# Kernel optimization log

Hardware: AMD Instinct MI355X
Metric: run time of the kernel (lower is better)

## Reference

```python
import jax, jax.numpy as jnp
import numpy as np
from jax import lax


def setup_inputs() -> dict:
    key = jax.random.key(0)
    ks = jax.random.split(key, 8)
    B, H, W = 1, 128, 128

    def rnd(k, shape, fan_in):
        return jax.random.normal(k, shape, dtype=jnp.float32) / np.float32(np.sqrt(fan_in))

    return {
        "x": jax.random.normal(ks[0], (B, 1, H, W), dtype=jnp.float32),
        "z": jax.random.uniform(ks[1], (B, 1), dtype=jnp.float32),
        "w_conv1": rnd(ks[2], (16, 1, 9, 9), 81),
        "b_conv1": jnp.zeros((16,), jnp.float32),
        "w_conv2": rnd(ks[3], (16, 16, 5, 5), 16 * 25),
        "b_conv2": jnp.zeros((16,), jnp.float32),
        "w_fc1": rnd(ks[4], (1024, 128), 1024),
        "b_fc1": jnp.zeros((128,), jnp.float32),
        "w_pose": rnd(ks[5], (1, 16), 1),
        "b_pose": jnp.zeros((16,), jnp.float32),
        "w_fc2": rnd(ks[6], (144, 1), 144),
        "b_fc2": jnp.zeros((1,), jnp.float32),
    }


_DN = ("NCHW", "OIHW", "NCHW")  # conv dimension numbers
_P = 32  # GQ-CNN patch size


def _maxpool2(h):
    return lax.reduce_window(h, -jnp.inf, lax.max, (1, 1, 2, 2), (1, 1, 2, 2), "VALID")


def _gqcnn(patches, z_rep, w_conv1, b_conv1, w_conv2, b_conv2,
           w_fc1, b_fc1, w_pose, b_pose, w_fc2, b_fc2):
    # patches: [N,1,32,32], z_rep: [N,1] -> quality [N,1]
    h = jax.nn.relu(lax.conv_general_dilated(patches, w_conv1, (1, 1), "SAME",
                                             dimension_numbers=_DN)
                    + b_conv1[None, :, None, None])
    h = _maxpool2(h)  # [N,16,16,16]
    h = jax.nn.relu(lax.conv_general_dilated(h, w_conv2, (1, 1), "SAME",
                                             dimension_numbers=_DN)
                    + b_conv2[None, :, None, None])
    h = _maxpool2(h)  # [N,16,8,8]
    flat = h.reshape(h.shape[0], -1)  # [N,1024]
    f = jax.nn.relu(flat @ w_fc1 + b_fc1)      # [N,128]
    p = jax.nn.relu(z_rep @ w_pose + b_pose)   # [N,16]
    return jnp.concatenate([f, p], axis=1) @ w_fc2 + b_fc2  # [N,1]


def reference(x, z, w_conv1, b_conv1, w_conv2, b_conv2,
              w_fc1, b_fc1, w_pose, b_pose, w_fc2, b_fc2):
    B, _, H, W = x.shape
    Hp, Wp = H - _P, W - _P  # loop ranges in the original: range(H-32), range(W-32)
    # Batched patch extraction replaces the O(H*W) Python loop.
    pat = lax.conv_general_dilated_patches(x, (_P, _P), (1, 1), "VALID")  # [B,1024,H-31,W-31]
    pat = pat[:, :, :Hp, :Wp]
    pat = jnp.transpose(pat, (0, 2, 3, 1)).reshape(B * Hp * Wp, 1, _P, _P)
    z_rep = jnp.repeat(z, Hp * Wp, axis=0)  # matches [B,Hp,Wp] flattening order
    q = _gqcnn(pat, z_rep, w_conv1, b_conv1, w_conv2, b_conv2,
               w_fc1, b_fc1, w_pose, b_pose, w_fc2, b_fc2)  # [N,1]
    half = _P // 2
    heat = jnp.zeros_like(x).at[:, :, half:H - half, half:W - half].set(
        q.reshape(B, 1, Hp, Wp))
    return heat
```

## Files before the change

kernel.cpp:

```cpp
#include <hip/hip_runtime.h>

typedef __attribute__((ext_vector_type(8))) short short8;
typedef __attribute__((ext_vector_type(4))) float f32x4;
typedef unsigned short u16;

__device__ __forceinline__ u16 f2bf(float f) {
    unsigned u = __builtin_bit_cast(unsigned, f);
    unsigned r = u + 0x7fffu + ((u >> 16) & 1u);
    return (u16)(r >> 16);
}
__device__ __forceinline__ unsigned pkbf(float lo, float hi) {
    unsigned r;
    asm("v_cvt_pk_bf16_f32 %0, %1, %2" : "=v"(r) : "v"(lo), "v"(hi));
    return r;
}

__global__ __launch_bounds__(256) void k0_prep(
    const float* __restrict__ z, const float* __restrict__ w1,
    const float* __restrict__ w2, const float* __restrict__ wfc1,
    const float* __restrict__ wpose, const float* __restrict__ bpose,
    const float* __restrict__ wfc2, const float* __restrict__ bfc2,
    float* __restrict__ out, u16* __restrict__ w1p, u16* __restrict__ w2p,
    u16* __restrict__ fc1T, float* __restrict__ cst)
{
    int gt = blockIdx.x * 256 + threadIdx.x;
    out[gt] = 0.f;

    if (gt < 2560) {
        int l = (gt >> 3) & 63, j = gt & 7, s = gt >> 9;
        int o = l & 15, bq = l >> 4;
        u16 v = 0;
        if (bq < 3) {
            int dx = bq * 4 + (j & 3);
            int dy = -1;
            if (s < 4) dy = 2 * s + (j >> 2);
            else if (j < 4) dy = 8;
            if (dy >= 0 && dx <= 8) v = f2bf(w1[o * 81 + dy * 9 + dx]);
        }
        w1p[gt] = v;
    }
    if (gt < 6656) {
        int l = (gt >> 3) & 63, j = gt & 7, s = gt >> 9;
        int o = l & 15, bq = l >> 4;
        int dy, dx, c8; bool valid = true;
        if (s < 5)       { dy = s;     dx = bq >> 1;       c8 = bq & 1; }
        else if (s < 10) { dy = s - 5; dx = 2 + (bq >> 1); c8 = bq & 1; }
        else { dy = (s - 10) + 3 * (bq & 1); dx = 4; c8 = bq >> 1; valid = (dy <= 4); }
        int ci = c8 * 8 + j;
        w2p[gt] = valid ? f2bf(w2[o * 400 + ci * 25 + dy * 5 + dx]) : (u16)0;
    }
    {
        int base = gt * 8;
        int n = base >> 10, kk = base & 1023;
        short8 v;
        #pragma unroll
        for (int j = 0; j < 8; ++j) v[j] = (short)f2bf(wfc1[(kk + j) * 128 + n]);
        *(short8*)&fc1T[base] = v;
    }
    if (gt == 0) {
        float zz = z[0];
        float s = bfc2[0];
        for (int j = 0; j < 16; ++j) {
            float p = fmaxf(zz * wpose[j] + bpose[j], 0.f);
            s += p * wfc2[128 + j];
        }
        *cst = s;
    }
}

__global__ __launch_bounds__(256, 4) void k1_feat(
    const float* __restrict__ x, const u16* __restrict__ w1p,
    const u16* __restrict__ w2p, const float* __restrict__ b1g,
    const float* __restrict__ b2g, u16* __restrict__ feat)
{
    __shared__ unsigned s2[40 * 44];
    __shared__ u16 s_h1p[20 * 20 * 24];
    __shared__ unsigned s_feat[512];

    const int tid = threadIdx.x;
    const int lane = tid & 63;
    const int wv = tid >> 6;
    const int mm = lane & 15;
    const int bq = lane >> 4;
    const int blk = blockIdx.x;
    const int py = blk / 96, px = blk % 96;

    {
        uint4 z4 = {0, 0, 0, 0};
        for (int i = tid; i < 152; i += 256) {
            int dst;
            if (i < 88) { int r8 = i / 11, c4 = i % 11;
                          int row = (r8 < 4) ? r8 : 32 + r8; dst = row * 11 + c4; }
            else        { int j = i - 88; dst = (4 + (j >> 1)) * 11 + 9 + (j & 1); }
            ((uint4*)s2)[dst] = z4;
        }
        for (int i = tid; i < 1728; i += 256) {
            int yx, d;
            if (i < 960) { int r = i / 240, off = i - r * 240;
                           int y = (r < 2) ? r : 16 + r;
                           yx = y * 20 + off / 12; d = off % 12; }
            else { int j = i - 960; int yy = 2 + j / 48; int rest = j % 48;
                   int xs = rest / 12; d = rest % 12;
                   int xx = (xs < 2) ? xs : 16 + xs; yx = yy * 20 + xx; }
            ((unsigned*)s_h1p)[yx * 12 + d] = 0;
        }
    }

    short8 w1f[5], w2f[13];
    #pragma unroll
    for (int s = 0; s < 5; ++s) w1f[s] = *(const short8*)&w1p[(s * 64 + lane) * 8];
    #pragma unroll
    for (int s = 0; s < 13; ++s) w2f[s] = *(const short8*)&w2p[(s * 64 + lane) * 8];
    const float bias1 = b1g[mm], bias2 = b2g[mm];

    for (int task = tid; task < 288; task += 256) {
        int ir = task / 9, g = task - ir * 9;
        int ic0 = g * 4 - 4;
        const float* xr = x + (py + ir) * 128 + px;
        float v[5];
        #pragma unroll
        for (int vi = 0; vi < 5; ++vi) {
            int ic = ic0 + vi;
            v[vi] = (ic >= 0 && ic < 32) ? xr[ic] : 0.f;
        }
        uint4 w;
        w.x = pkbf(v[0], v[1]);
        w.y = pkbf(v[1], v[2]);
        w.z = pkbf(v[2], v[3]);
        w.w = pkbf(v[3], v[4]);
        *(uint4*)&s2[(4 + ir) * 44 + g * 4] = w;
    }
    __syncthreads();

    union F { short8 s; unsigned u[4]; };
    const int dxq = (bq == 3) ? 0 : bq;

    for (int qi = 0; qi < 4; ++qi) {
        int q = wv + qi * 4;
        for (int h = 0; h < 2; ++h) {
            const unsigned* pb = &s2[(2 * q) * 44 + h * 16 + mm + dxq * 4];
            f32x4 accA = {0, 0, 0, 0}, accB = {0, 0, 0, 0};
            #pragma unroll
            for (int s = 0; s < 5; ++s) {
                F a, b;
                const unsigned* ra = pb + 2 * s * 44;
                a.u[0] = ra[0];  a.u[1] = ra[2];
                a.u[2] = ra[44]; a.u[3] = ra[46];
                const int blo = (s < 4) ? (2 * s + 1) * 44 : 9 * 44;
                const int bhi = (s < 4) ? (2 * s + 2) * 44 : 8 * 44;
                b.u[0] = pb[blo];     b.u[1] = pb[blo + 2];
                b.u[2] = pb[bhi];     b.u[3] = pb[bhi + 2];
                accA = __builtin_amdgcn_mfma_f32_16x16x32_bf16(a.s, w1f[s], accA, 0, 0, 0);
                accB = __builtin_amdgcn_mfma_f32_16x16x32_bf16(b.s, w1f[s], accB, 0, 0, 0);
            }
            float vr0, vr1;
            {
                float a0 = fmaxf(fmaxf(accA[0], accA[1]), fmaxf(accB[0], accB[1]));
                vr0 = fmaxf(a0 + bias1, 0.f);
                float a1 = fmaxf(fmaxf(accA[2], accA[3]), fmaxf(accB[2], accB[3]));
                vr1 = fmaxf(a1 + bias1, 0.f);
            }
            unsigned pw = pkbf(vr0, vr1);
            int pc = h * 8 + (bq << 1);
            int cb = ((2 + q) * 20 + (2 + pc)) * 24 + mm;
            s_h1p[cb] = (u16)pw;
            s_h1p[cb + 24] = (u16)(pw >> 16);
        }
    }
    __syncthreads();

    for (int pi = 0; pi < 2; ++pi) {
        int q = wv + pi * 4;
        int c8s = (bq & 1) * 8;
        int baseA = ((2 * q) * 20 + mm + (bq >> 1)) * 24 + c8s;
        int baseB = baseA + 2 * 24;
        int c8C = (bq >> 1) * 8;
        int yC0 = 2 * q + 3 * (bq & 1);
        short8 A6[6], B6[6], C4[4];
        #pragma unroll
        for (int i = 0; i < 6; ++i) {
            A6[i] = *(const short8*)&s_h1p[baseA + i * 480];
            B6[i] = *(const short8*)&s_h1p[baseB + i * 480];
        }
        #pragma unroll
        for (int i = 0; i < 4; ++i) {
            int y = yC0 + i; if (y > 19) y = 19;
            C4[i] = *(const short8*)&s_h1p[(y * 20 + mm + 4) * 24 + c8C];
        }
        f32x4 accA = {0, 0, 0, 0}, accB = {0, 0, 0, 0};
        #pragma unroll
        for (int s = 0; s < 5; ++s) {
            accA = __builtin_amdgcn_mfma_f32_16x16x32_bf16(A6[s],     w2f[s], accA, 0, 0, 0);
            accB = __builtin_amdgcn_mfma_f32_16x16x32_bf16(A6[s + 1], w2f[s], accB, 0, 0, 0);
        }
        #pragma unroll
        for (int s = 0; s < 5; ++s) {
            accA = __builtin_amdgcn_mfma_f32_16x16x32_bf16(B6[s],     w2f[5 + s], accA, 0, 0, 0);
            accB = __builtin_amdgcn_mfma_f32_16x16x32_bf16(B6[s + 1], w2f[5 + s], accB, 0, 0, 0);
        }
        #pragma unroll
        for (int s = 0; s < 3; ++s) {
            accA = __builtin_amdgcn_mfma_f32_16x16x32_bf16(C4[s],     w2f[10 + s], accA, 0, 0, 0);
            accB = __builtin_amdgcn_mfma_f32_16x16x32_bf16(C4[s + 1], w2f[10 + s], accB, 0, 0, 0);
        }
        float v0, v1;
        {
            float a = fmaxf(fmaxf(accA[0], accA[1]), fmaxf(accB[0], accB[1]));
            v0 = fmaxf(a + bias2, 0.f);
            float b = fmaxf(fmaxf(accA[2], accA[3]), fmaxf(accB[2], accB[3]));
            v1 = fmaxf(b + bias2, 0.f);
        }
        unsigned dwv = pkbf(v0, v1);
        s_feat[mm * 32 + ((q * 4 + bq) ^ mm)] = dwv;
    }
    __syncthreads();

    {
        int ci = tid >> 4, t = tid & 15;
        uint2 v;
        v.x = s_feat[ci * 32 + ((2 * t) ^ ci)];
        v.y = s_feat[ci * 32 + ((2 * t + 1) ^ ci)];
        *(uint2*)&feat[blk * 1024 + tid * 4] = v;
    }
}

__global__ __launch_bounds__(256) void k2_fc(
    const u16* __restrict__ feat, const u16* __restrict__ fc1T,
    const float* __restrict__ bfc1, const float* __restrict__ wfc2,
    const float* __restrict__ cst, float* __restrict__ out)
{
    __shared__ u16 sA[64 * 136];
    __shared__ u16 sB[128 * 136];
    const int tid = threadIdx.x;
    const int lane = tid & 63;
    const int wv = tid >> 6;
    const int mm = lane & 15;
    const int bq = lane >> 4;
    const int p0 = blockIdx.x * 64;

    f32x4 acc[8];
    #pragma unroll
    for (int i = 0; i < 8; ++i) acc[i] = (f32x4){0, 0, 0, 0};

    for (int kt = 0; kt < 8; ++kt) {
        for (int i = tid; i < 1024; i += 256) {
            int row = i >> 4, ch = i & 15;
            *(short8*)&sA[row * 136 + ch * 8] =
                *(const short8*)&feat[(p0 + row) * 1024 + kt * 128 + ch * 8];
        }
        for (int i = tid; i < 2048; i += 256) {
            int row = i >> 4, ch = i & 15;
            *(short8*)&sB[row * 136 + ch * 8] =
                *(const short8*)&fc1T[row * 1024 + kt * 128 + ch * 8];
        }
        __syncthreads();
        #pragma unroll
        for (int ks = 0; ks < 4; ++ks) {
            short8 aF = *(const short8*)&sA[(wv * 16 + mm) * 136 + ks * 32 + bq * 8];
            #pragma unroll
            for (int nt = 0; nt < 8; ++nt) {
                short8 bF = *(const short8*)&sB[(nt * 16 + mm) * 136 + ks * 32 + bq * 8];
                acc[nt] = __builtin_amdgcn_mfma_f32_16x16x32_bf16(aF, bF, acc[nt], 0, 0, 0);
            }
        }
        __syncthreads();
    }

    const float cpose = *cst;
    float qs[4] = {0, 0, 0, 0};
    #pragma unroll
    for (int nt = 0; nt < 8; ++nt) {
        int n = nt * 16 + mm;
        float bb = bfc1[n], wf = wfc2[n];
        #pragma unroll
        for (int r = 0; r < 4; ++r) {
            float f = fmaxf(acc[nt][r] + bb, 0.f);
            qs[r] += f * wf;
        }
    }
    #pragma unroll
    for (int r = 0; r < 4; ++r) {
        float v = qs[r];
        v += __shfl_xor(v, 1);
        v += __shfl_xor(v, 2);
        v += __shfl_xor(v, 4);
        v += __shfl_xor(v, 8);
        qs[r] = v;
    }
    if (mm == 0) {
        #pragma unroll
        for (int r = 0; r < 4; ++r) {
            int p = p0 + wv * 16 + bq * 4 + r;
            int qy = p / 96, qx = p % 96;
            out[(16 + qy) * 128 + (16 + qx)] = qs[r] + cpose;
        }
    }
}

extern "C" void kernel_launch(void* const* d_in, const int* in_sizes, int n_in,
                              void* d_out, int out_size, void* d_ws, size_t ws_size,
                              hipStream_t stream)
{
    const float* x     = (const float*)d_in[0];
    const float* z     = (const float*)d_in[1];
    const float* w1    = (const float*)d_in[2];
    const float* b1    = (const float*)d_in[3];
    const float* w2    = (const float*)d_in[4];
    const float* b2    = (const float*)d_in[5];
    const float* wfc1  = (const float*)d_in[6];
    const float* bfc1  = (const float*)d_in[7];
    const float* wpose = (const float*)d_in[8];
    const float* bpose = (const float*)d_in[9];
    const float* wfc2  = (const float*)d_in[10];
    const float* bfc2  = (const float*)d_in[11];
    float* out = (float*)d_out;

    char* ws = (char*)d_ws;
    u16*   w1p  = (u16*)(ws + 0);
    u16*   w2p  = (u16*)(ws + 8192);
    float* cst  = (float*)(ws + 22528);
    u16*   fc1T = (u16*)(ws + 24576);
    u16*   feat = (u16*)(ws + 294912);

    hipLaunchKernelGGL(k0_prep, dim3(64), dim3(256), 0, stream,
                       z, w1, w2, wfc1, wpose, bpose, wfc2, bfc2,
                       out, w1p, w2p, fc1T, cst);
    hipLaunchKernelGGL(k1_feat, dim3(9216), dim3(256), 0, stream,
                       x, w1p, w2p, b1, b2, feat);
    hipLaunchKernelGGL(k2_fc, dim3(144), dim3(256), 0, stream,
                       feat, fc1T, bfc1, wfc2, cst, out);
}
```

Measured before the change: 115.8 us.

## Interleave independent MFMA chains in conv stages and simplify halo zeroing

Conv1 now processes both column halves together and conv2 both row tasks together, so four independent MFMA accumulator chains are interleaved and LDS loads for the next step are issued ahead of the MFMAs. The halo zeroing of the padded conv1 buffer becomes a flat vectorized clear of the whole buffer. Occupancy hint drops from 4 to 2 blocks per CU to allow more registers. The aim is to hide MFMA dependency latency and LDS latency, at the cost of higher register pressure and possibly fewer resident waves.

Result: faster. 107.6 us (-7.1%).

```diff
diff --git a/kernel.cpp b/kernel.cpp
--- a/kernel.cpp
+++ b/kernel.cpp
@@ -68,7 +68,7 @@
     }
 }
 
-__global__ __launch_bounds__(256, 4) void k1_feat(
+__global__ __launch_bounds__(256, 2) void k1_feat(
     const float* __restrict__ x, const u16* __restrict__ w1p,
     const u16* __restrict__ w2p, const float* __restrict__ b1g,
     const float* __restrict__ b2g, u16* __restrict__ feat)
@@ -94,16 +94,7 @@
             else        { int j = i - 88; dst = (4 + (j >> 1)) * 11 + 9 + (j & 1); }
             ((uint4*)s2)[dst] = z4;
         }
-        for (int i = tid; i < 1728; i += 256) {
-            int yx, d;
-            if (i < 960) { int r = i / 240, off = i - r * 240;
-                           int y = (r < 2) ? r : 16 + r;
-                           yx = y * 20 + off / 12; d = off % 12; }
-            else { int j = i - 960; int yy = 2 + j / 48; int rest = j % 48;
-                   int xs = rest / 12; d = rest % 12;
-                   int xx = (xs < 2) ? xs : 16 + xs; yx = yy * 20 + xx; }
-            ((unsigned*)s_h1p)[yx * 12 + d] = 0;
-        }
+        for (int i = tid; i < 1200; i += 256) ((uint4*)s_h1p)[i] = z4;
     }
 
     short8 w1f[5], w2f[13];
@@ -137,27 +128,37 @@
 
     for (int qi = 0; qi < 4; ++qi) {
         int q = wv + qi * 4;
+        const unsigned* pb0 = &s2[(2 * q) * 44 + mm + dxq * 4];
+        const unsigned* pb1 = pb0 + 16;
+        f32x4 ac0 = {0, 0, 0, 0}, ac1 = {0, 0, 0, 0};
+        f32x4 ac2 = {0, 0, 0, 0}, ac3 = {0, 0, 0, 0};
+        #pragma unroll
+        for (int s = 0; s < 5; ++s) {
+            const int ra  = 2 * s * 44;
+            const int blo = (s < 4) ? (2 * s + 1) * 44 : 9 * 44;
+            const int bhi = (s < 4) ? (2 * s + 2) * 44 : 8 * 44;
+            F fa0, fa1, fb0, fb1;
+            fa0.u[0] = pb0[ra];      fa0.u[1] = pb0[ra + 2];
+            fa0.u[2] = pb0[ra + 44]; fa0.u[3] = pb0[ra + 46];
+            fa1.u[0] = pb1[ra];      fa1.u[1] = pb1[ra + 2];
+            fa1.u[2] = pb1[ra + 44]; fa1.u[3] = pb1[ra + 46];
+            fb0.u[0] = pb0[blo];     fb0.u[1] = pb0[blo + 2];
+            fb0.u[2] = pb0[bhi];     fb0.u[3] = pb0[bhi + 2];
+            fb1.u[0] = pb1[blo];     fb1.u[1] = pb1[blo + 2];
+            fb1.u[2] = pb1[bhi];     fb1.u[3] = pb1[bhi + 2];
+            ac0 = __builtin_amdgcn_mfma_f32_16x16x32_bf16(fa0.s, w1f[s], ac0, 0, 0, 0);
+            ac2 = __builtin_amdgcn_mfma_f32_16x16x32_bf16(fa1.s, w1f[s], ac2, 0, 0, 0);
+            ac1 = __builtin_amdgcn_mfma_f32_16x16x32_bf16(fb0.s, w1f[s], ac1, 0, 0, 0);
+            ac3 = __builtin_amdgcn_mfma_f32_16x16x32_bf16(fb1.s, w1f[s], ac3, 0, 0, 0);
+        }
+        #pragma unroll
         for (int h = 0; h < 2; ++h) {
-            const unsigned* pb = &s2[(2 * q) * 44 + h * 16 + mm + dxq * 4];
-            f32x4 accA = {0, 0, 0, 0}, accB = {0, 0, 0, 0};
-            #pragma unroll
-            for (int s = 0; s < 5; ++s) {
-                F a, b;
-                const unsigned* ra = pb + 2 * s * 44;
-                a.u[0] = ra[0];  a.u[1] = ra[2];
-                a.u[2] = ra[44]; a.u[3] = ra[46];
-                const int blo = (s < 4) ? (2 * s + 1) * 44 : 9 * 44;
-                const int bhi = (s < 4) ? (2 * s + 2) * 44 : 8 * 44;
-                b.u[0] = pb[blo];     b.u[1] = pb[blo + 2];
-                b.u[2] = pb[bhi];     b.u[3] = pb[bhi + 2];
-                accA = __builtin_amdgcn_mfma_f32_16x16x32_bf16(a.s, w1f[s], accA, 0, 0, 0);
-                accB = __builtin_amdgcn_mfma_f32_16x16x32_bf16(b.s, w1f[s], accB, 0, 0, 0);
-            }
+            f32x4 aA = h ? ac2 : ac0, aB = h ? ac3 : ac1;
             float vr0, vr1;
             {
-                float a0 = fmaxf(fmaxf(accA[0], accA[1]), fmaxf(accB[0], accB[1]));
+                float a0 = fmaxf(fmaxf(aA[0], aA[1]), fmaxf(aB[0], aB[1]));
                 vr0 = fmaxf(a0 + bias1, 0.f);
-                float a1 = fmaxf(fmaxf(accA[2], accA[3]), fmaxf(accB[2], accB[3]));
+                float a1 = fmaxf(fmaxf(aA[2], aA[3]), fmaxf(aB[2], aB[3]));
                 vr1 = fmaxf(a1 + bias1, 0.f);
             }
             unsigned pw = pkbf(vr0, vr1);
@@ -169,49 +170,74 @@
     }
     __syncthreads();
 
-    for (int pi = 0; pi < 2; ++pi) {
-        int q = wv + pi * 4;
-        int c8s = (bq & 1) * 8;
-        int baseA = ((2 * q) * 20 + mm + (bq >> 1)) * 24 + c8s;
-        int baseB = baseA + 2 * 24;
-        int c8C = (bq >> 1) * 8;
-        int yC0 = 2 * q + 3 * (bq & 1);
-        short8 A6[6], B6[6], C4[4];
-        #pragma unroll
-        for (int i = 0; i < 6; ++i) {
-            A6[i] = *(const short8*)&s_h1p[baseA + i * 480];
-            B6[i] = *(const short8*)&s_h1p[baseB + i * 480];
-        }
-        #pragma unroll
-        for (int i = 0; i < 4; ++i) {
-            int y = yC0 + i; if (y > 19) y = 19;
-            C4[i] = *(const short8*)&s_h1p[(y * 20 + mm + 4) * 24 + c8C];
-        }
-        f32x4 accA = {0, 0, 0, 0}, accB = {0, 0, 0, 0};
+    {
+        const int q0 = wv, q1 = wv + 4;
+        const int c8s = (bq & 1) * 8;
+        const int baseA0 = ((2 * q0) * 20 + mm + (bq >> 1)) * 24 + c8s;
+        const int baseA1 = ((2 * q1) * 20 + mm + (bq >> 1)) * 24 + c8s;
+        const int baseB0 = baseA0 + 2 * 24;
+        const int baseB1 = baseA1 + 2 * 24;
+        const int c8C = (bq >> 1) * 8;
+        const int yC0 = 2 * q0 + 3 * (bq & 1);
+        const int yC1 = 2 * q1 + 3 * (bq & 1);
+        f32x4 p0A = {0, 0, 0, 0}, p0B = {0, 0, 0, 0};
+        f32x4 p1A = {0, 0, 0, 0}, p1B = {0, 0, 0, 0};
+
+        short8 a0 = *(const short8*)&s_h1p[baseA0];
+        short8 a1 = *(const short8*)&s_h1p[baseA1];
         #pragma unroll
         for (int s = 0; s < 5; ++s) {
-            accA = __builtin_amdgcn_mfma_f32_16x16x32_bf16(A6[s],     w2f[s], accA, 0, 0, 0);
-            accB = __builtin_amdgcn_mfma_f32_16x16x32_bf16(A6[s + 1], w2f[s], accB, 0, 0, 0);
-        }
+            short8 n0 = *(const short8*)&s_h1p[baseA0 + (s + 1) * 480];
+            short8 n1 = *(const short8*)&s_h1p[baseA1 + (s + 1) * 480];
+            p0A = __builtin_amdgcn_mfma_f32_16x16x32_bf16(a0, w2f[s], p0A, 0, 0, 0);
+            p1A = __builtin_amdgcn_mfma_f32_16x16x32_bf16(a1, w2f[s], p1A, 0, 0, 0);
+            p0B = __builtin_amdgcn_mfma_f32_16x16x32_bf16(n0, w2f[s], p0B, 0, 0, 0);
+            p1B = __builtin_amdgcn_mfma_f32_16x16x32_bf16(n1, w2f[s], p1B, 0, 0, 0);
+            a0 = n0; a1 = n1;
+        }
+        a0 = *(const short8*)&s_h1p[baseB0];
+        a1 = *(const short8*)&s_h1p[baseB1];
         #pragma unroll
         for (int s = 0; s < 5; ++s) {
-            accA = __builtin_amdgcn_mfma_f32_16x16x32_bf16(B6[s],     w2f[5 + s], accA, 0, 0, 0);
-            accB = __builtin_amdgcn_mfma_f32_16x16x32_bf16(B6[s + 1], w2f[5 + s], accB, 0, 0, 0);
+            short8 n0 = *(const short8*)&s_h1p[baseB0 + (s + 1) * 480];
+            short8 n1 = *(const short8*)&s_h1p[baseB1 + (s + 1) * 480];
+            p0A = __builtin_amdgcn_mfma_f32_16x16x32_bf16(a0, w2f[5 + s], p0A, 0, 0, 0);
+            p1A = __builtin_amdgcn_mfma_f32_16x16x32_bf16(a1, w2f[5 + s], p1A, 0, 0, 0);
+            p0B = __builtin_amdgcn_mfma_f32_16x16x32_bf16(n0, w2f[5 + s], p0B, 0, 0, 0);
+            p1B = __builtin_amdgcn_mfma_f32_16x16x32_bf16(n1, w2f[5 + s], p1B, 0, 0, 0);
+            a0 = n0; a1 = n1;
+        }
+        {
+            int y00 = yC0, y10 = (yC1 > 19) ? 19 : yC1;
+            a0 = *(const short8*)&s_h1p[(y00 * 20 + mm + 4) * 24 + c8C];
+            a1 = *(const short8*)&s_h1p[(y10 * 20 + mm + 4) * 24 + c8C];
         }
         #pragma unroll
         for (int s = 0; s < 3; ++s) {
-            accA = __builtin_amdgcn_mfma_f32_16x16x32_bf16(C4[s],     w2f[10 + s], accA, 0, 0, 0);
-            accB = __builtin_amdgcn_mfma_f32_16x16x32_bf16(C4[s + 1], w2f[10 + s], accB, 0, 0, 0);
-        }
-        float v0, v1;
-        {
-            float a = fmaxf(fmaxf(accA[0], accA[1]), fmaxf(accB[0], accB[1]));
-            v0 = fmaxf(a + bias2, 0.f);
-            float b = fmaxf(fmaxf(accA[2], accA[3]), fmaxf(accB[2], accB[3]));
-            v1 = fmaxf(b + bias2, 0.f);
-        }
-        unsigned dwv = pkbf(v0, v1);
-        s_feat[mm * 32 + ((q * 4 + bq) ^ mm)] = dwv;
+            int y0n = yC0 + s + 1; if (y0n > 19) y0n = 19;
+            int y1n = yC1 + s + 1; if (y1n > 19) y1n = 19;
+            short8 n0 = *(const short8*)&s_h1p[(y0n * 20 + mm + 4) * 24 + c8C];
+            short8 n1 = *(const short8*)&s_h1p[(y1n * 20 + mm + 4) * 24 + c8C];
+            p0A = __builtin_amdgcn_mfma_f32_16x16x32_bf16(a0, w2f[10 + s], p0A, 0, 0, 0);
+            p1A = __builtin_amdgcn_mfma_f32_16x16x32_bf16(a1, w2f[10 + s], p1A, 0, 0, 0);
+            p0B = __builtin_amdgcn_mfma_f32_16x16x32_bf16(n0, w2f[10 + s], p0B, 0, 0, 0);
+            p1B = __builtin_amdgcn_mfma_f32_16x16x32_bf16(n1, w2f[10 + s], p1B, 0, 0, 0);
+            a0 = n0; a1 = n1;
+        }
+        #pragma unroll
+        for (int pi = 0; pi < 2; ++pi) {
+            f32x4 aA = pi ? p1A : p0A, aB = pi ? p1B : p0B;
+            int q = pi ? q1 : q0;
+            float v0, v1;
+            {
+                float a = fmaxf(fmaxf(aA[0], aA[1]), fmaxf(aB[0], aB[1]));
+                v0 = fmaxf(a + bias2, 0.f);
+                float b = fmaxf(fmaxf(aA[2], aA[3]), fmaxf(aB[2], aB[3]));
+                v1 = fmaxf(b + bias2, 0.f);
+            }
+            unsigned dwv = pkbf(v0, v1);
+            s_feat[mm * 32 + ((q * 4 + bq) ^ mm)] = dwv;
+        }
     }
     __syncthreads();
 
```
